# Optimization experiments

Measured on AMD Instinct MI355X. Metric: run time of the kernel, lower is better.

Reference implementation:

```python
import jax, jax.numpy as jnp
import numpy as np

QMAX = 127.0  # int8 symmetric
EPS = 1e-8

def _quant_dequant(v, axis):
    # symmetric int8 fake-quant along `axis` (per-row for weights, per-token for acts)
    scale = jnp.max(jnp.abs(v), axis=axis, keepdims=True) / QMAX
    scale = jnp.maximum(scale, EPS)
    q = jnp.clip(jnp.round(v / scale), -QMAX, QMAX)
    return q * scale

def _ste(v, axis):
    # straight-through estimator: identity gradient through quantization
    return v + jax.lax.stop_gradient(_quant_dequant(v, axis) - v)

def setup_inputs() -> dict:
    key = jax.random.key(0)
    k1, k2, k3 = jax.random.split(key, 3)
    H, I = 2048, 5632
    x = jax.random.normal(k1, (4, 2048, H), dtype=jnp.float32)
    # nn.Linear weight layout: [out_features, in_features]
    w_gate_up = jax.random.normal(k2, (2 * I, H), dtype=jnp.float32) * (H ** -0.5)
    w_down = jax.random.normal(k3, (H, I), dtype=jnp.float32) * (I ** -0.5)
    return {"x": x, "w_gate_up": w_gate_up, "w_down": w_down}

def reference(x, w_gate_up, w_down):
    I = w_down.shape[1]
    # QLinear #1: quantize act per-token, weight per-out-channel, dequant matmul
    xq = _ste(x, axis=-1)                       # [B,S,H]
    w1q = _ste(w_gate_up, axis=-1)              # [2I,H]
    gate_up = jnp.einsum('bsh,oh->bso', xq, w1q)  # [B,S,2I]
    gate, up = gate_up[..., :I], gate_up[..., I:]
    h = jax.nn.silu(gate) * up                  # SwiGLU, [B,S,I]
    # QLinear #2
    hq = _ste(h, axis=-1)
    w2q = _ste(w_down, axis=-1)                 # [H,I]
    return jnp.einsum('bsi,oi->bso', hq, w2q)   # [B,S,H]
```

## Files before the change

### kernel.cpp

```cpp
#include <hip/hip_runtime.h>
#include <hip/hip_bf16.h>
#include <stdint.h>

#define H_DIM 2048
#define I_DIM 5632
#define M_DIM 8192
#define N1_DIM (2 * I_DIM)
#define NBN1 (I_DIM / 128)
#define NPART (NBN1 * 4)

typedef __attribute__((ext_vector_type(4))) int i32x4;

__device__ __forceinline__ void gload16(const void* g, void* l) {
  __builtin_amdgcn_global_load_lds(
      reinterpret_cast<const __attribute__((address_space(1))) uint32_t*>(
          reinterpret_cast<uintptr_t>(g)),
      reinterpret_cast<__attribute__((address_space(3))) uint32_t*>(
          reinterpret_cast<uintptr_t>(l)),
      16, 0, 0);
}

__device__ __forceinline__ i32x4 ds_read128(uint32_t addr) {
  i32x4 d;
  asm volatile("s_mov_b32 m0, -1\n\tds_read_b128 %0, %1"
               : "=v"(d)
               : "v"(addr));
  return d;
}

#define MEMF() asm volatile("" ::: "memory")
#define BAR()                      \
  do {                             \
    MEMF();                        \
    __builtin_amdgcn_s_barrier();  \
    MEMF();                        \
  } while (0)
#define SCHEDB() __builtin_amdgcn_sched_barrier(0)

__global__ __launch_bounds__(256) void quant_rows_f32(
    const float* __restrict__ in, int8_t* __restrict__ q,
    float* __restrict__ scl, int rowlen) {
  const int row = blockIdx.x;
  const int tid = threadIdx.x;
  const float* rp = in + (size_t)row * rowlen;
  float m = 0.f;
  for (int i = tid * 4; i < rowlen; i += 1024) {
    const float4 v = *reinterpret_cast<const float4*>(rp + i);
    m = fmaxf(m, fmaxf(fmaxf(fabsf(v.x), fabsf(v.y)),
                       fmaxf(fabsf(v.z), fabsf(v.w))));
  }
#pragma unroll
  for (int o = 32; o; o >>= 1) m = fmaxf(m, __shfl_xor(m, o));
  __shared__ float wm[4];
  if ((tid & 63) == 0) wm[tid >> 6] = m;
  __syncthreads();
  m = fmaxf(fmaxf(wm[0], wm[1]), fmaxf(wm[2], wm[3]));
  const float scale = fmaxf(m / 127.0f, 1e-8f);
  const float inv = 1.0f / scale;
  if (tid == 0) scl[row] = scale;
  int8_t* qp = q + (size_t)row * rowlen;
  for (int i = tid * 4; i < rowlen; i += 1024) {
    const float4 v = *reinterpret_cast<const float4*>(rp + i);
    const int a = (int)rintf(fminf(fmaxf(v.x * inv, -127.f), 127.f));
    const int b = (int)rintf(fminf(fmaxf(v.y * inv, -127.f), 127.f));
    const int c = (int)rintf(fminf(fmaxf(v.z * inv, -127.f), 127.f));
    const int d = (int)rintf(fminf(fmaxf(v.w * inv, -127.f), 127.f));
    *reinterpret_cast<int*>(qp + i) =
        (a & 255) | ((b & 255) << 8) | ((c & 255) << 16) | (d << 24);
  }
}

__global__ __launch_bounds__(256) void quant_h_rows(
    const __hip_bfloat16* __restrict__ h, const float* __restrict__ hpart,
    int8_t* __restrict__ q, float* __restrict__ scl) {
  const int row = blockIdx.x;
  const int tid = threadIdx.x;
  float m = (tid < NPART) ? hpart[(size_t)row * NPART + tid] : 0.f;
#pragma unroll
  for (int o = 32; o; o >>= 1) m = fmaxf(m, __shfl_xor(m, o));
  __shared__ float wm[4];
  if ((tid & 63) == 0) wm[tid >> 6] = m;
  __syncthreads();
  m = fmaxf(fmaxf(wm[0], wm[1]), fmaxf(wm[2], wm[3]));
  const float scale = fmaxf(m / 127.0f, 1e-8f);
  const float inv = 1.0f / scale;
  if (tid == 0) scl[row] = scale;
  const __hip_bfloat16* rp = h + (size_t)row * I_DIM;
  int8_t* qp = q + (size_t)row * I_DIM;
  for (int i = tid * 8; i < I_DIM; i += 2048) {
    const uint4 v = *reinterpret_cast<const uint4*>(rp + i);
    const uint32_t w[4] = {v.x, v.y, v.z, v.w};
    int pk0 = 0, pk1 = 0;
#pragma unroll
    for (int j = 0; j < 8; ++j) {
      const float f =
          __uint_as_float(((w[j >> 1] >> ((j & 1) * 16)) & 0xffffu) << 16);
      const int qv = (int)rintf(fminf(fmaxf(f * inv, -127.f), 127.f));
      if (j < 4) pk0 |= (qv & 255) << ((j & 3) * 8);
      else       pk1 |= (qv & 255) << ((j & 3) * 8);
    }
    *reinterpret_cast<int2*>(qp + i) = make_int2(pk0, pk1);
  }
}

__global__ __launch_bounds__(512, 2) void gemm1_silu(
    const int8_t* __restrict__ qx, const float* __restrict__ sx,
    const int8_t* __restrict__ qw, const float* __restrict__ sw,
    __hip_bfloat16* __restrict__ h, float* __restrict__ hpart) {
  __shared__ int8_t lds[131072];
  const int tid = threadIdx.x;
  const int lane = tid & 63;
  const int wid = tid >> 6;
  const int wr = wid >> 2, wc = wid & 3;
  const int c16 = lane & 15, kq = lane >> 4, r7 = lane & 7, lr = lane >> 3;
  const int sslot = ((lane & 7) ^ lr) << 4;
  const int sl0 = (kq ^ r7) << 4;
  const int sl1 = ((4 + kq) ^ r7) << 4;

  const int nwg = gridDim.x;
  const int id = blockIdx.x;
  const int swz = (id & 7) * (nwg >> 3) + (id >> 3);
  const int bm = swz / NBN1, bn = swz % NBN1;

  const int xrow = wid * 8 + lr;
  const int fx = (xrow & ~31) | ((xrow & 15) << 1) | ((xrow >> 4) & 1);

  const size_t goffA = (size_t)(bm * 256 + xrow) * H_DIM + sslot;
  const size_t goffG = (size_t)(bn * 128 + fx) * H_DIM + sslot;
  const size_t goffU = goffG + (size_t)I_DIM * H_DIM;
  const int ldsAw = wid * 8 * 128;
  const int ldsBw = 65536 + wid * 8 * 128;

  const uint32_t L = (uint32_t)(uintptr_t)(void*)&lds[0];
  const uint32_t aB0 = L + (wr * 64 + c16) * 128 + sl0;
  const uint32_t aB1 = L + (wr * 64 + c16) * 128 + sl1;
  const uint32_t bB0 = L + 65536 + (wc * 32 + c16) * 128 + sl0;
  const uint32_t bB1 = L + 65536 + (wc * 32 + c16) * 128 + sl1;

  i32x4 acc[2][4][2][2] = {};

#define STAGE_A1(half, t)                                                      \
  do {                                                                         \
    const int _b = ((t) & 1) * 32768;                                          \
    _Pragma("unroll") for (int ld = 0; ld < 2; ++ld)                           \
        gload16(qx + goffA + (size_t)((half)*128 + ld * 64) * H_DIM +          \
                    (size_t)(t) * 128,                                         \
                lds + _b + ldsAw + ((half)*128 + ld * 64) * 128);              \
  } while (0)

#define STAGE_B1(half, t)                                                      \
  do {                                                                         \
    const int _b = ((t) & 1) * 32768;                                          \
    const int8_t* _s = (half) ? (qw + goffU) : (qw + goffG);                   \
    _Pragma("unroll") for (int ld = 0; ld < 2; ++ld)                           \
        gload16(_s + (size_t)(ld * 64) * H_DIM + (size_t)(t) * 128,            \
                lds + _b + ldsBw + ((half)*128 + ld * 64) * 128);              \
  } while (0)

#define RD_A(MH)                                                               \
  do {                                                                         \
    _Pragma("unroll") for (int m = 0; m < 4; ++m) {                            \
      a[MH][m][0] = ds_read128(ab0 + (MH)*16384 + m * 2048);                   \
      a[MH][m][1] = ds_read128(ab1 + (MH)*16384 + m * 2048);                   \
    }                                                                          \
  } while (0)

#define RD_B(NH)                                                               \
  do {                                                                         \
    _Pragma("unroll") for (int n = 0; n < 2; ++n) {                            \
      b[NH][n][0] = ds_read128(bb0 + (NH)*16384 + n * 2048);                   \
      b[NH][n][1] = ds_read128(bb1 + (NH)*16384 + n * 2048);                   \
    }                                                                          \
  } while (0)

#define MFMA_Q(MH, NH)                                                         \
  do {                                                                         \
    __builtin_amdgcn_s_setprio(1);                                             \
    _Pragma("unroll") for (int kk = 0; kk < 2; ++kk)                           \
        _Pragma("unroll") for (int m = 0; m < 4; ++m)                          \
            _Pragma("unroll") for (int n = 0; n < 2; ++n) acc[MH][m][NH][n] =  \
        __builtin_amdgcn_mfma_i32_16x16x64_i8(a[MH][m][kk], b[NH][n][kk],      \
                                              acc[MH][m][NH][n], 0, 0, 0);     \
    __builtin_amdgcn_s_setprio(0);                                             \
  } while (0)

  const int KT = H_DIM / 128;
  STAGE_A1(0, 0); STAGE_B1(0, 0); STAGE_A1(1, 0); STAGE_B1(1, 0);
  STAGE_A1(0, 1); STAGE_B1(0, 1);
  asm volatile("s_waitcnt vmcnt(4)" ::: "memory");
  BAR();

#pragma unroll 1
  for (int t = 0; t < KT; ++t) {
    const int cb = (t & 1) * 32768;
    const uint32_t ab0 = aB0 + cb, ab1 = aB1 + cb;
    const uint32_t bb0 = bB0 + cb, bb1 = bB1 + cb;
    i32x4 a[2][4][2], b[2][2][2];
    RD_B(0); RD_A(0); RD_B(1);
    MEMF();
    if (t + 1 < KT) { STAGE_A1(1, t + 1); STAGE_B1(1, t + 1); }
    BAR();
    asm volatile("s_waitcnt lgkmcnt(4)" ::: "memory");
    SCHEDB();
    MFMA_Q(0, 0);
    asm volatile("s_waitcnt lgkmcnt(0)" ::: "memory");
    SCHEDB();
    MFMA_Q(0, 1);
    BAR();
    RD_A(1);
    MEMF();
    if (t + 2 < KT) { STAGE_A1(0, t + 2); STAGE_B1(0, t + 2); }
    BAR();
    asm volatile("s_waitcnt lgkmcnt(0)" ::: "memory");
    SCHEDB();
    MFMA_Q(1, 0);
    MFMA_Q(1, 1);
    if (t + 2 < KT) asm volatile("s_waitcnt vmcnt(4)" ::: "memory");
    else            asm volatile("s_waitcnt vmcnt(0)" ::: "memory");
    BAR();
  }

  const int row0 = bm * 256 + wr * 64 + kq * 4;
  const int colb = bn * 128 + wc * 32 + 2 * c16;
#pragma unroll
  for (int mh = 0; mh < 2; ++mh) {
#pragma unroll
    for (int m = 0; m < 4; ++m) {
#pragma unroll
      for (int r = 0; r < 4; ++r) {
        const int row = row0 + mh * 128 + m * 16 + r;
        const float sxr = sx[row];
        float hv[2];
#pragma unroll
        for (int n = 0; n < 2; ++n) {
          const int col = colb + n;
          const float g = (float)acc[mh][m][0][n][r] * (sxr * sw[col]);
          const float u = (float)acc[mh][m][1][n][r] * (sxr * sw[I_DIM + col]);
          hv[n] = g / (1.f + __expf(-g)) * u;
        }
        const uint32_t p0 = __bfloat16_as_ushort(__float2bfloat16(hv[0]));
        const uint32_t p1 = __bfloat16_as_ushort(__float2bfloat16(hv[1]));
        *reinterpret_cast<uint32_t*>(&h[(size_t)row * I_DIM + colb]) =
            p0 | (p1 << 16);
        float rmax = fmaxf(fabsf(hv[0]), fabsf(hv[1]));
#pragma unroll
        for (int o = 1; o < 16; o <<= 1)
          rmax = fmaxf(rmax, __shfl_xor(rmax, o));
        if (c16 == 0)
          hpart[(size_t)row * NPART + bn * 4 + wc] = rmax;
      }
    }
  }
}

__global__ __launch_bounds__(512, 2) void gemm2(
    const int8_t* __restrict__ qh, const float* __restrict__ sh,
    const int8_t* __restrict__ qw, const float* __restrict__ sw,
    float* __restrict__ out) {
  __shared__ int8_t lds[131072];
  const int tid = threadIdx.x;
  const int lane = tid & 63;
  const int wid = tid >> 6;
  const int wr = wid >> 2, wc = wid & 3;
  const int c16 = lane & 15, kq = lane >> 4, r7 = lane & 7, lr = lane >> 3;
  const int sslot = ((lane & 7) ^ lr) << 4;
  const int sl0 = (kq ^ r7) << 4;
  const int sl1 = ((4 + kq) ^ r7) << 4;

  const int nwg = gridDim.x;
  const int id = blockIdx.x;
  const int swz = (id & 7) * (nwg >> 3) + (id >> 3);
  const int NBN = H_DIM / 256;
  const int bm = swz / NBN, bn = swz % NBN;

  const size_t goffA = (size_t)(bm * 256 + wid * 8 + lr) * I_DIM + sslot;
  const size_t goffB = (size_t)(bn * 256 + wid * 8 + lr) * I_DIM + sslot;
  const int ldsAw = wid * 8 * 128;
  const int ldsBw = 65536 + wid * 8 * 128;

  const uint32_t L = (uint32_t)(uintptr_t)(void*)&lds[0];
  const uint32_t aB0 = L + (wr * 64 + c16) * 128 + sl0;
  const uint32_t aB1 = L + (wr * 64 + c16) * 128 + sl1;
  const uint32_t bB0 = L + 65536 + (wc * 32 + c16) * 128 + sl0;
  const uint32_t bB1 = L + 65536 + (wc * 32 + c16) * 128 + sl1;

  i32x4 acc[2][4][2][2] = {};

#define STAGE_A2(half, t)                                                      \
  do {                                                                         \
    const int _b = ((t) & 1) * 32768;                                          \
    _Pragma("unroll") for (int ld = 0; ld < 2; ++ld)                           \
        gload16(qh + goffA + (size_t)((half)*128 + ld * 64) * I_DIM +          \
                    (size_t)(t) * 128,                                         \
                lds + _b + ldsAw + ((half)*128 + ld * 64) * 128);              \
  } while (0)

#define STAGE_B2(half, t)                                                      \
  do {                                                                         \
    const int _b = ((t) & 1) * 32768;                                          \
    _Pragma("unroll") for (int ld = 0; ld < 2; ++ld)                           \
        gload16(qw + goffB + (size_t)((half)*128 + ld * 64) * I_DIM +          \
                    (size_t)(t) * 128,                                         \
                lds + _b + ldsBw + ((half)*128 + ld * 64) * 128);              \
  } while (0)

  const int KT = I_DIM / 128;
  STAGE_A2(0, 0); STAGE_B2(0, 0); STAGE_A2(1, 0); STAGE_B2(1, 0);
  STAGE_A2(0, 1); STAGE_B2(0, 1);
  asm volatile("s_waitcnt vmcnt(4)" ::: "memory");
  BAR();

#pragma unroll 1
  for (int t = 0; t < KT; ++t) {
    const int cb = (t & 1) * 32768;
    const uint32_t ab0 = aB0 + cb, ab1 = aB1 + cb;
    const uint32_t bb0 = bB0 + cb, bb1 = bB1 + cb;
    i32x4 a[2][4][2], b[2][2][2];
    RD_B(0); RD_A(0); RD_B(1);
    MEMF();
    if (t + 1 < KT) { STAGE_A2(1, t + 1); STAGE_B2(1, t + 1); }
    BAR();
    asm volatile("s_waitcnt lgkmcnt(4)" ::: "memory");
    SCHEDB();
    MFMA_Q(0, 0);
    asm volatile("s_waitcnt lgkmcnt(0)" ::: "memory");
    SCHEDB();
    MFMA_Q(0, 1);
    BAR();
    RD_A(1);
    MEMF();
    if (t + 2 < KT) { STAGE_A2(0, t + 2); STAGE_B2(0, t + 2); }
    BAR();
    asm volatile("s_waitcnt lgkmcnt(0)" ::: "memory");
    SCHEDB();
    MFMA_Q(1, 0);
    MFMA_Q(1, 1);
    if (t + 2 < KT) asm volatile("s_waitcnt vmcnt(4)" ::: "memory");
    else            asm volatile("s_waitcnt vmcnt(0)" ::: "memory");
    BAR();
  }

  const int row0 = bm * 256 + wr * 64 + kq * 4;
  const int col0 = bn * 256 + wc * 32 + c16;
#pragma unroll
  for (int mh = 0; mh < 2; ++mh) {
#pragma unroll
    for (int m = 0; m < 4; ++m) {
#pragma unroll
      for (int r = 0; r < 4; ++r) {
        const int row = row0 + mh * 128 + m * 16 + r;
        const float shr = sh[row];
#pragma unroll
        for (int nh = 0; nh < 2; ++nh) {
#pragma unroll
          for (int n = 0; n < 2; ++n) {
            const int col = col0 + nh * 128 + n * 16;
            out[(size_t)row * H_DIM + col] =
                (float)acc[mh][m][nh][n][r] * (shr * sw[col]);
          }
        }
      }
    }
  }
}

extern "C" void kernel_launch(void* const* d_in, const int* in_sizes, int n_in,
                              void* d_out, int out_size, void* d_ws, size_t ws_size,
                              hipStream_t stream) {
  (void)in_sizes; (void)n_in; (void)out_size; (void)ws_size;
  const float* x  = (const float*)d_in[0];
  const float* w1 = (const float*)d_in[1];
  const float* w2 = (const float*)d_in[2];
  float* out = (float*)d_out;

  size_t off = 0;
  auto alloc = [&](size_t n) {
    void* p = (char*)d_ws + off;
    off += (n + 255) & ~(size_t)255;
    return p;
  };
  int8_t* qx  = (int8_t*)alloc((size_t)M_DIM * H_DIM);
  int8_t* qw1 = (int8_t*)alloc((size_t)N1_DIM * H_DIM);
  int8_t* qw2 = (int8_t*)alloc((size_t)H_DIM * I_DIM);
  int8_t* qh  = (int8_t*)alloc((size_t)M_DIM * I_DIM);
  __hip_bfloat16* hb = (__hip_bfloat16*)alloc((size_t)M_DIM * I_DIM * 2);
  float* sx    = (float*)alloc((size_t)M_DIM * 4);
  float* sw1   = (float*)alloc((size_t)N1_DIM * 4);
  float* sw2   = (float*)alloc((size_t)H_DIM * 4);
  float* shs   = (float*)alloc((size_t)M_DIM * 4);
  float* hpart = (float*)alloc((size_t)M_DIM * NPART * 4);

  quant_rows_f32<<<M_DIM, 256, 0, stream>>>(x, qx, sx, H_DIM);
  quant_rows_f32<<<N1_DIM, 256, 0, stream>>>(w1, qw1, sw1, H_DIM);
  quant_rows_f32<<<H_DIM, 256, 0, stream>>>(w2, qw2, sw2, I_DIM);
  gemm1_silu<<<(M_DIM / 256) * NBN1, 512, 0, stream>>>(
      qx, sx, qw1, sw1, hb, hpart);
  quant_h_rows<<<M_DIM, 256, 0, stream>>>(hb, hpart, qh, shs);
  gemm2<<<(M_DIM / 256) * (H_DIM / 256), 512, 0, stream>>>(
      qh, shs, qw2, sw2, out);
}
```

Before: 408.6 us.

## Software-pipeline LDS fragment reads across k-tiles in int8 GEMM main loops

```diff
diff --git a/kernel.cpp b/kernel.cpp
--- a/kernel.cpp
+++ b/kernel.cpp
@@ -103,6 +103,77 @@
   }
 }
 
+#define RD_A(MH, BUF)                                                          \
+  do {                                                                         \
+    _Pragma("unroll") for (int m = 0; m < 4; ++m) {                            \
+      a[MH][m][0] = ds_read128(aB0 + (BUF) + (MH)*16384 + m * 2048);           \
+      a[MH][m][1] = ds_read128(aB1 + (BUF) + (MH)*16384 + m * 2048);           \
+    }                                                                          \
+  } while (0)
+
+#define RD_B(NH, BUF)                                                          \
+  do {                                                                         \
+    _Pragma("unroll") for (int n = 0; n < 2; ++n) {                            \
+      b[NH][n][0] = ds_read128(bB0 + (BUF) + (NH)*16384 + n * 2048);           \
+      b[NH][n][1] = ds_read128(bB1 + (BUF) + (NH)*16384 + n * 2048);           \
+    }                                                                          \
+  } while (0)
+
+#define MFMA_Q(MH, NH)                                                         \
+  do {                                                                         \
+    __builtin_amdgcn_s_setprio(1);                                             \
+    _Pragma("unroll") for (int kk = 0; kk < 2; ++kk)                           \
+        _Pragma("unroll") for (int m = 0; m < 4; ++m)                          \
+            _Pragma("unroll") for (int n = 0; n < 2; ++n) acc[MH][m][NH][n] =  \
+        __builtin_amdgcn_mfma_i32_16x16x64_i8(a[MH][m][kk], b[NH][n][kk],      \
+                                              acc[MH][m][NH][n], 0, 0, 0);     \
+    __builtin_amdgcn_s_setprio(0);                                             \
+  } while (0)
+
+#define KTILE_BODY(SA, SB)                                                     \
+  do {                                                                         \
+    const int cb = (t & 1) * 32768;                                            \
+    const int nb = cb ^ 32768;                                                 \
+                                                                      \
+    SCHEDB();                                                                  \
+    RD_B(1, cb);                                                               \
+    MEMF();                                                                    \
+    if (t + 1 < KT) SA(1, t + 1);                                              \
+    asm volatile("s_waitcnt lgkmcnt(4)" ::: "memory");                         \
+    SCHEDB();                                                                  \
+    MFMA_Q(0, 0);                                                              \
+    BAR();                                                                     \
+                                                                      \
+    SCHEDB();                                                                  \
+    RD_A(1, cb);                                                               \
+    MEMF();                                                                    \
+    if (t + 1 < KT) SB(1, t + 1);                                              \
+    asm volatile("s_waitcnt lgkmcnt(8)" ::: "memory");                         \
+    SCHEDB();                                                                  \
+    MFMA_Q(0, 1);                                                              \
+    BAR();                                                                     \
+                                                                      \
+    SCHEDB();                                                                  \
+    if (t + 2 < KT) SA(0, t + 2);                                              \
+    asm volatile("s_waitcnt lgkmcnt(0)" ::: "memory");                         \
+    SCHEDB();                                                                  \
+    MFMA_Q(1, 0);                                                              \
+    if (t + 2 < KT) asm volatile("s_waitcnt vmcnt(6)" ::: "memory");           \
+    else            asm volatile("s_waitcnt vmcnt(0)" ::: "memory");           \
+    BAR();                                                                     \
+                                                                      \
+    SCHEDB();                                                                  \
+    if (t + 1 < KT) { RD_A(0, nb); RD_B(0, nb); }                              \
+    MEMF();                                                                    \
+    if (t + 2 < KT) SB(0, t + 2);                                              \
+    MFMA_Q(1, 1);                                                              \
+    if (t + 1 < KT) {                                                          \
+      if (t + 2 < KT) asm volatile("s_waitcnt vmcnt(4)" ::: "memory");         \
+      else            asm volatile("s_waitcnt vmcnt(0)" ::: "memory");         \
+    }                                                                          \
+    BAR();                                                                     \
+  } while (0)
+
 __global__ __launch_bounds__(512, 2) void gemm1_silu(
     const int8_t* __restrict__ qx, const float* __restrict__ sx,
     const int8_t* __restrict__ qw, const float* __restrict__ sw,
@@ -138,6 +209,7 @@
   const uint32_t bB1 = L + 65536 + (wc * 32 + c16) * 128 + sl1;
 
   i32x4 acc[2][4][2][2] = {};
+  i32x4 a[2][4][2], b[2][2][2];
 
 #define STAGE_A1(half, t)                                                      \
   do {                                                                         \
@@ -157,67 +229,17 @@
                 lds + _b + ldsBw + ((half)*128 + ld * 64) * 128);              \
   } while (0)
 
-#define RD_A(MH)                                                               \
-  do {                                                                         \
-    _Pragma("unroll") for (int m = 0; m < 4; ++m) {                            \
-      a[MH][m][0] = ds_read128(ab0 + (MH)*16384 + m * 2048);                   \
-      a[MH][m][1] = ds_read128(ab1 + (MH)*16384 + m * 2048);                   \
-    }                                                                          \
-  } while (0)
-
-#define RD_B(NH)                                                               \
-  do {                                                                         \
-    _Pragma("unroll") for (int n = 0; n < 2; ++n) {                            \
-      b[NH][n][0] = ds_read128(bb0 + (NH)*16384 + n * 2048);                   \
-      b[NH][n][1] = ds_read128(bb1 + (NH)*16384 + n * 2048);                   \
-    }                                                                          \
-  } while (0)
-
-#define MFMA_Q(MH, NH)                                                         \
-  do {                                                                         \
-    __builtin_amdgcn_s_setprio(1);                                             \
-    _Pragma("unroll") for (int kk = 0; kk < 2; ++kk)                           \
-        _Pragma("unroll") for (int m = 0; m < 4; ++m)                          \
-            _Pragma("unroll") for (int n = 0; n < 2; ++n) acc[MH][m][NH][n] =  \
-        __builtin_amdgcn_mfma_i32_16x16x64_i8(a[MH][m][kk], b[NH][n][kk],      \
-                                              acc[MH][m][NH][n], 0, 0, 0);     \
-    __builtin_amdgcn_s_setprio(0);                                             \
-  } while (0)
-
   const int KT = H_DIM / 128;
   STAGE_A1(0, 0); STAGE_B1(0, 0); STAGE_A1(1, 0); STAGE_B1(1, 0);
   STAGE_A1(0, 1); STAGE_B1(0, 1);
   asm volatile("s_waitcnt vmcnt(4)" ::: "memory");
   BAR();
+  RD_A(0, 0); RD_B(0, 0);
+  MEMF();
 
 #pragma unroll 1
   for (int t = 0; t < KT; ++t) {
-    const int cb = (t & 1) * 32768;
-    const uint32_t ab0 = aB0 + cb, ab1 = aB1 + cb;
-    const uint32_t bb0 = bB0 + cb, bb1 = bB1 + cb;
-    i32x4 a[2][4][2], b[2][2][2];
-    RD_B(0); RD_A(0); RD_B(1);
-    MEMF();
-    if (t + 1 < KT) { STAGE_A1(1, t + 1); STAGE_B1(1, t + 1); }
-    BAR();
-    asm volatile("s_waitcnt lgkmcnt(4)" ::: "memory");
-    SCHEDB();
-    MFMA_Q(0, 0);
-    asm volatile("s_waitcnt lgkmcnt(0)" ::: "memory");
-    SCHEDB();
-    MFMA_Q(0, 1);
-    BAR();
-    RD_A(1);
-    MEMF();
-    if (t + 2 < KT) { STAGE_A1(0, t + 2); STAGE_B1(0, t + 2); }
-    BAR();
-    asm volatile("s_waitcnt lgkmcnt(0)" ::: "memory");
-    SCHEDB();
-    MFMA_Q(1, 0);
-    MFMA_Q(1, 1);
-    if (t + 2 < KT) asm volatile("s_waitcnt vmcnt(4)" ::: "memory");
-    else            asm volatile("s_waitcnt vmcnt(0)" ::: "memory");
-    BAR();
+    KTILE_BODY(STAGE_A1, STAGE_B1);
   }
 
   const int row0 = bm * 256 + wr * 64 + kq * 4;
@@ -285,6 +307,7 @@
   const uint32_t bB1 = L + 65536 + (wc * 32 + c16) * 128 + sl1;
 
   i32x4 acc[2][4][2][2] = {};
+  i32x4 a[2][4][2], b[2][2][2];
 
 #define STAGE_A2(half, t)                                                      \
   do {                                                                         \
@@ -309,35 +332,12 @@
   STAGE_A2(0, 1); STAGE_B2(0, 1);
   asm volatile("s_waitcnt vmcnt(4)" ::: "memory");
   BAR();
+  RD_A(0, 0); RD_B(0, 0);
+  MEMF();
 
 #pragma unroll 1
   for (int t = 0; t < KT; ++t) {
-    const int cb = (t & 1) * 32768;
-    const uint32_t ab0 = aB0 + cb, ab1 = aB1 + cb;
-    const uint32_t bb0 = bB0 + cb, bb1 = bB1 + cb;
-    i32x4 a[2][4][2], b[2][2][2];
-    RD_B(0); RD_A(0); RD_B(1);
-    MEMF();
-    if (t + 1 < KT) { STAGE_A2(1, t + 1); STAGE_B2(1, t + 1); }
-    BAR();
-    asm volatile("s_waitcnt lgkmcnt(4)" ::: "memory");
-    SCHEDB();
-    MFMA_Q(0, 0);
-    asm volatile("s_waitcnt lgkmcnt(0)" ::: "memory");
-    SCHEDB();
-    MFMA_Q(0, 1);
-    BAR();
-    RD_A(1);
-    MEMF();
-    if (t + 2 < KT) { STAGE_A2(0, t + 2); STAGE_B2(0, t + 2); }
-    BAR();
-    asm volatile("s_waitcnt lgkmcnt(0)" ::: "memory");
-    SCHEDB();
-    MFMA_Q(1, 0);
-    MFMA_Q(1, 1);
-    if (t + 2 < KT) asm volatile("s_waitcnt vmcnt(4)" ::: "memory");
-    else            asm volatile("s_waitcnt vmcnt(0)" ::: "memory");
-    BAR();
+    KTILE_BODY(STAGE_A2, STAGE_B2);
   }
 
   const int row0 = bm * 256 + wr * 64 + kq * 4;
```

After: 403.3 us. About the same (-1.3%).

## Make gemm1 persistent with cross-tile prefetch and restage both GEMM main loops

Applied to the files above, without the earlier changes.

```diff
diff --git a/kernel.cpp b/kernel.cpp
--- a/kernel.cpp
+++ b/kernel.cpp
@@ -8,6 +8,8 @@
 #define N1_DIM (2 * I_DIM)
 #define NBN1 (I_DIM / 128)
 #define NPART (NBN1 * 4)
+#define NT1 ((M_DIM / 256) * NBN1)
+#define G1_GRID 256
 
 typedef __attribute__((ext_vector_type(4))) int i32x4;
 
@@ -103,6 +105,33 @@
   }
 }
 
+#define RD_A(MH, BUF)                                                          \
+  do {                                                                         \
+    _Pragma("unroll") for (int m = 0; m < 4; ++m) {                            \
+      a[MH][m][0] = ds_read128(aB0 + (BUF) + (MH)*16384 + m * 2048);           \
+      a[MH][m][1] = ds_read128(aB1 + (BUF) + (MH)*16384 + m * 2048);           \
+    }                                                                          \
+  } while (0)
+
+#define RD_B(NH, BUF)                                                          \
+  do {                                                                         \
+    _Pragma("unroll") for (int n = 0; n < 2; ++n) {                            \
+      b[NH][n][0] = ds_read128(bB0 + (BUF) + (NH)*16384 + n * 2048);           \
+      b[NH][n][1] = ds_read128(bB1 + (BUF) + (NH)*16384 + n * 2048);           \
+    }                                                                          \
+  } while (0)
+
+#define MFMA_Q(MH, NH)                                                         \
+  do {                                                                         \
+    __builtin_amdgcn_s_setprio(1);                                             \
+    _Pragma("unroll") for (int kk = 0; kk < 2; ++kk)                           \
+        _Pragma("unroll") for (int m = 0; m < 4; ++m)                          \
+            _Pragma("unroll") for (int n = 0; n < 2; ++n) acc[MH][m][NH][n] =  \
+        __builtin_amdgcn_mfma_i32_16x16x64_i8(a[MH][m][kk], b[NH][n][kk],      \
+                                              acc[MH][m][NH][n], 0, 0, 0);     \
+    __builtin_amdgcn_s_setprio(0);                                             \
+  } while (0)
+
 __global__ __launch_bounds__(512, 2) void gemm1_silu(
     const int8_t* __restrict__ qx, const float* __restrict__ sx,
     const int8_t* __restrict__ qw, const float* __restrict__ sw,
@@ -117,17 +146,9 @@
   const int sl0 = (kq ^ r7) << 4;
   const int sl1 = ((4 + kq) ^ r7) << 4;
 
-  const int nwg = gridDim.x;
-  const int id = blockIdx.x;
-  const int swz = (id & 7) * (nwg >> 3) + (id >> 3);
-  const int bm = swz / NBN1, bn = swz % NBN1;
-
   const int xrow = wid * 8 + lr;
   const int fx = (xrow & ~31) | ((xrow & 15) << 1) | ((xrow >> 4) & 1);
 
-  const size_t goffA = (size_t)(bm * 256 + xrow) * H_DIM + sslot;
-  const size_t goffG = (size_t)(bn * 128 + fx) * H_DIM + sslot;
-  const size_t goffU = goffG + (size_t)I_DIM * H_DIM;
   const int ldsAw = wid * 8 * 128;
   const int ldsBw = 65536 + wid * 8 * 128;
 
@@ -137,119 +158,148 @@
   const uint32_t bB0 = L + 65536 + (wc * 32 + c16) * 128 + sl0;
   const uint32_t bB1 = L + 65536 + (wc * 32 + c16) * 128 + sl1;
 
-  i32x4 acc[2][4][2][2] = {};
-
-#define STAGE_A1(half, t)                                                      \
-  do {                                                                         \
-    const int _b = ((t) & 1) * 32768;                                          \
+  const int KT = H_DIM / 128;
+
+#define STG_A(P, half, vv)                                                     \
+  do {                                                                         \
+    const int _b = ((vv) & 1) * 32768;                                         \
+    const int _t = (vv) & 15;                                                  \
     _Pragma("unroll") for (int ld = 0; ld < 2; ++ld)                           \
-        gload16(qx + goffA + (size_t)((half)*128 + ld * 64) * H_DIM +          \
-                    (size_t)(t) * 128,                                         \
+        gload16((P) + (size_t)((half)*128 + ld * 64) * H_DIM +                 \
+                    (size_t)_t * 128,                                          \
                 lds + _b + ldsAw + ((half)*128 + ld * 64) * 128);              \
   } while (0)
 
-#define STAGE_B1(half, t)                                                      \
-  do {                                                                         \
-    const int _b = ((t) & 1) * 32768;                                          \
-    const int8_t* _s = (half) ? (qw + goffU) : (qw + goffG);                   \
+#define STG_B(P, half, vv)                                                     \
+  do {                                                                         \
+    const int _b = ((vv) & 1) * 32768;                                         \
+    const int _t = (vv) & 15;                                                  \
     _Pragma("unroll") for (int ld = 0; ld < 2; ++ld)                           \
-        gload16(_s + (size_t)(ld * 64) * H_DIM + (size_t)(t) * 128,            \
+        gload16((P) + (size_t)(ld * 64) * H_DIM + (size_t)_t * 128,            \
                 lds + _b + ldsBw + ((half)*128 + ld * 64) * 128);              \
   } while (0)
 
-#define RD_A(MH)                                                               \
-  do {                                                                         \
-    _Pragma("unroll") for (int m = 0; m < 4; ++m) {                            \
-      a[MH][m][0] = ds_read128(ab0 + (MH)*16384 + m * 2048);                   \
-      a[MH][m][1] = ds_read128(ab1 + (MH)*16384 + m * 2048);                   \
-    }                                                                          \
-  } while (0)
-
-#define RD_B(NH)                                                               \
-  do {                                                                         \
-    _Pragma("unroll") for (int n = 0; n < 2; ++n) {                            \
-      b[NH][n][0] = ds_read128(bb0 + (NH)*16384 + n * 2048);                   \
-      b[NH][n][1] = ds_read128(bb1 + (NH)*16384 + n * 2048);                   \
-    }                                                                          \
-  } while (0)
-
-#define MFMA_Q(MH, NH)                                                         \
-  do {                                                                         \
-    __builtin_amdgcn_s_setprio(1);                                             \
-    _Pragma("unroll") for (int kk = 0; kk < 2; ++kk)                           \
-        _Pragma("unroll") for (int m = 0; m < 4; ++m)                          \
-            _Pragma("unroll") for (int n = 0; n < 2; ++n) acc[MH][m][NH][n] =  \
-        __builtin_amdgcn_mfma_i32_16x16x64_i8(a[MH][m][kk], b[NH][n][kk],      \
-                                              acc[MH][m][NH][n], 0, 0, 0);     \
-    __builtin_amdgcn_s_setprio(0);                                             \
-  } while (0)
-
-  const int KT = H_DIM / 128;
-  STAGE_A1(0, 0); STAGE_B1(0, 0); STAGE_A1(1, 0); STAGE_B1(1, 0);
-  STAGE_A1(0, 1); STAGE_B1(0, 1);
+  int v = blockIdx.x;
+  int swz = (v & 7) * (NT1 / 8) + (v >> 3);
+  int bm_c = swz / NBN1, bn_c = swz % NBN1;
+  const int8_t* pAc = qx + (size_t)(bm_c * 256 + xrow) * H_DIM + sslot;
+  const int8_t* pGc = qw + (size_t)(bn_c * 128 + fx) * H_DIM + sslot;
+  const int8_t* pUc = pGc + (size_t)I_DIM * H_DIM;
+
+  i32x4 acc[2][4][2][2];
+  i32x4 a[2][4][2], b[2][2][2];
+
+  STG_A(pAc, 0, 0); STG_B(pGc, 0, 0);
+  STG_A(pAc, 1, 0); STG_B(pUc, 1, 0);
+  STG_A(pAc, 0, 1); STG_B(pGc, 0, 1);
   asm volatile("s_waitcnt vmcnt(4)" ::: "memory");
   BAR();
 
 #pragma unroll 1
-  for (int t = 0; t < KT; ++t) {
-    const int cb = (t & 1) * 32768;
-    const uint32_t ab0 = aB0 + cb, ab1 = aB1 + cb;
-    const uint32_t bb0 = bB0 + cb, bb1 = bB1 + cb;
-    i32x4 a[2][4][2], b[2][2][2];
-    RD_B(0); RD_A(0); RD_B(1);
+  for (; v < NT1; v += G1_GRID) {
+    const bool last = (v + G1_GRID >= NT1);
+    const int vn = last ? v : v + G1_GRID;
+    const int swzn = (vn & 7) * (NT1 / 8) + (vn >> 3);
+    const int bm_n = swzn / NBN1, bn_n = swzn % NBN1;
+    const int8_t* pAn = qx + (size_t)(bm_n * 256 + xrow) * H_DIM + sslot;
+    const int8_t* pGn = qw + (size_t)(bn_n * 128 + fx) * H_DIM + sslot;
+    const int8_t* pUn = pGn + (size_t)I_DIM * H_DIM;
+
+    RD_A(0, 0); RD_B(0, 0);
     MEMF();
-    if (t + 1 < KT) { STAGE_A1(1, t + 1); STAGE_B1(1, t + 1); }
-    BAR();
-    asm volatile("s_waitcnt lgkmcnt(4)" ::: "memory");
-    SCHEDB();
-    MFMA_Q(0, 0);
-    asm volatile("s_waitcnt lgkmcnt(0)" ::: "memory");
-    SCHEDB();
-    MFMA_Q(0, 1);
-    BAR();
-    RD_A(1);
-    MEMF();
-    if (t + 2 < KT) { STAGE_A1(0, t + 2); STAGE_B1(0, t + 2); }
-    BAR();
-    asm volatile("s_waitcnt lgkmcnt(0)" ::: "memory");
-    SCHEDB();
-    MFMA_Q(1, 0);
-    MFMA_Q(1, 1);
-    if (t + 2 < KT) asm volatile("s_waitcnt vmcnt(4)" ::: "memory");
-    else            asm volatile("s_waitcnt vmcnt(0)" ::: "memory");
-    BAR();
-  }
-
-  const int row0 = bm * 256 + wr * 64 + kq * 4;
-  const int colb = bn * 128 + wc * 32 + 2 * c16;
-#pragma unroll
-  for (int mh = 0; mh < 2; ++mh) {
-#pragma unroll
-    for (int m = 0; m < 4; ++m) {
-#pragma unroll
-      for (int r = 0; r < 4; ++r) {
-        const int row = row0 + mh * 128 + m * 16 + r;
-        const float sxr = sx[row];
-        float hv[2];
-#pragma unroll
-        for (int n = 0; n < 2; ++n) {
-          const int col = colb + n;
-          const float g = (float)acc[mh][m][0][n][r] * (sxr * sw[col]);
-          const float u = (float)acc[mh][m][1][n][r] * (sxr * sw[I_DIM + col]);
-          hv[n] = g / (1.f + __expf(-g)) * u;
+
+#pragma unroll
+    for (int mh = 0; mh < 2; ++mh)
+#pragma unroll
+      for (int m = 0; m < 4; ++m)
+#pragma unroll
+        for (int nh = 0; nh < 2; ++nh)
+#pragma unroll
+          for (int n = 0; n < 2; ++n) acc[mh][m][nh][n] = i32x4{0, 0, 0, 0};
+
+#pragma unroll 1
+    for (int t = 0; t < KT; ++t) {
+      const int cb = (t & 1) * 32768;
+      const int nb = cb ^ 32768;
+      SCHEDB();
+      RD_B(1, cb);
+      MEMF();
+      if (t + 1 < KT)      STG_A(pAc, 1, t + 1);
+      else if (!last)      STG_A(pAn, 1, t + 1);
+      asm volatile("s_waitcnt lgkmcnt(4)" ::: "memory");
+      SCHEDB();
+      MFMA_Q(0, 0);
+      BAR();
+      SCHEDB();
+      RD_A(1, cb);
+      MEMF();
+      if (t + 1 < KT)      STG_B(pUc, 1, t + 1);
+      else if (!last)      STG_B(pUn, 1, t + 1);
+      asm volatile("s_waitcnt lgkmcnt(8)" ::: "memory");
+      SCHEDB();
+      MFMA_Q(0, 1);
+      BAR();
+      SCHEDB();
+      if (t + 2 < KT)      STG_A(pAc, 0, t + 2);
+      else if (!last)      STG_A(pAn, 0, t + 2);
+      asm volatile("s_waitcnt lgkmcnt(0)" ::: "memory");
+      SCHEDB();
+      MFMA_Q(1, 0);
+      if (t + 2 < KT || !last)
+        asm volatile("s_waitcnt vmcnt(6)" ::: "memory");
+      else
+        asm volatile("s_waitcnt vmcnt(0)" ::: "memory");
+      BAR();
+      SCHEDB();
+      if (t + 1 < KT) { RD_A(0, nb); RD_B(0, nb); }
+      MEMF();
+      if (t + 2 < KT)      STG_B(pGc, 0, t + 2);
+      else if (!last)      STG_B(pGn, 0, t + 2);
+      MFMA_Q(1, 1);
+      if (t + 1 < KT || !last) {
+        if (t + 2 < KT || !last)
+          asm volatile("s_waitcnt vmcnt(4)" ::: "memory");
+        else
+          asm volatile("s_waitcnt vmcnt(0)" ::: "memory");
+      }
+      BAR();
+    }
+
+    const int row0 = bm_c * 256 + wr * 64 + kq * 4;
+    const int colb = bn_c * 128 + wc * 32 + 2 * c16;
+#pragma unroll
+    for (int mh = 0; mh < 2; ++mh) {
+#pragma unroll
+      for (int m = 0; m < 4; ++m) {
+#pragma unroll
+        for (int r = 0; r < 4; ++r) {
+          const int row = row0 + mh * 128 + m * 16 + r;
+          const float sxr = sx[row];
+          float hv[2];
+#pragma unroll
+          for (int n = 0; n < 2; ++n) {
+            const int col = colb + n;
+            const float g = (float)acc[mh][m][0][n][r] * (sxr * sw[col]);
+            const float u =
+                (float)acc[mh][m][1][n][r] * (sxr * sw[I_DIM + col]);
+            hv[n] = g / (1.f + __expf(-g)) * u;
+          }
+          const uint32_t p0 = __bfloat16_as_ushort(__float2bfloat16(hv[0]));
+          const uint32_t p1 = __bfloat16_as_ushort(__float2bfloat16(hv[1]));
+          *reinterpret_cast<uint32_t*>(&h[(size_t)row * I_DIM + colb]) =
+              p0 | (p1 << 16);
+          float rmax = fmaxf(fabsf(hv[0]), fabsf(hv[1]));
+#pragma unroll
+          for (int o = 1; o < 16; o <<= 1)
+            rmax = fmaxf(rmax, __shfl_xor(rmax, o));
+          if (c16 == 0)
+            hpart[(size_t)row * NPART + bn_c * 4 + wc] = rmax;
         }
-        const uint32_t p0 = __bfloat16_as_ushort(__float2bfloat16(hv[0]));
-        const uint32_t p1 = __bfloat16_as_ushort(__float2bfloat16(hv[1]));
-        *reinterpret_cast<uint32_t*>(&h[(size_t)row * I_DIM + colb]) =
-            p0 | (p1 << 16);
-        float rmax = fmaxf(fabsf(hv[0]), fabsf(hv[1]));
-#pragma unroll
-        for (int o = 1; o < 16; o <<= 1)
-          rmax = fmaxf(rmax, __shfl_xor(rmax, o));
-        if (c16 == 0)
-          hpart[(size_t)row * NPART + bn * 4 + wc] = rmax;
       }
     }
+
+    bm_c = bm_n; bn_c = bn_n;
+    pAc = pAn; pGc = pGn; pUc = pUn;
   }
 }
 
@@ -285,6 +335,7 @@
   const uint32_t bB1 = L + 65536 + (wc * 32 + c16) * 128 + sl1;
 
   i32x4 acc[2][4][2][2] = {};
+  i32x4 a[2][4][2], b[2][2][2];
 
 #define STAGE_A2(half, t)                                                      \
   do {                                                                         \
@@ -309,34 +360,46 @@
   STAGE_A2(0, 1); STAGE_B2(0, 1);
   asm volatile("s_waitcnt vmcnt(4)" ::: "memory");
   BAR();
+  RD_A(0, 0); RD_B(0, 0);
+  MEMF();
 
 #pragma unroll 1
   for (int t = 0; t < KT; ++t) {
     const int cb = (t & 1) * 32768;
-    const uint32_t ab0 = aB0 + cb, ab1 = aB1 + cb;
-    const uint32_t bb0 = bB0 + cb, bb1 = bB1 + cb;
-    i32x4 a[2][4][2], b[2][2][2];
-    RD_B(0); RD_A(0); RD_B(1);
+    const int nb = cb ^ 32768;
+    SCHEDB();
+    RD_B(1, cb);
     MEMF();
-    if (t + 1 < KT) { STAGE_A2(1, t + 1); STAGE_B2(1, t + 1); }
+    if (t + 1 < KT) STAGE_A2(1, t + 1);
+    asm volatile("s_waitcnt lgkmcnt(4)" ::: "memory");
+    SCHEDB();
+    MFMA_Q(0, 0);
     BAR();
-    asm volatile("s_waitcnt lgkmcnt(4)" ::: "memory");
-    SCHEDB();
-    MFMA_Q(0, 0);
-    asm volatile("s_waitcnt lgkmcnt(0)" ::: "memory");
+    SCHEDB();
+    RD_A(1, cb);
+    MEMF();
+    if (t + 1 < KT) STAGE_B2(1, t + 1);
+    asm volatile("s_waitcnt lgkmcnt(8)" ::: "memory");
     SCHEDB();
     MFMA_Q(0, 1);
     BAR();
-    RD_A(1);
+    SCHEDB();
+    if (t + 2 < KT) STAGE_A2(0, t + 2);
+    asm volatile("s_waitcnt lgkmcnt(0)" ::: "memory");
+    SCHEDB();
+    MFMA_Q(1, 0);
+    if (t + 2 < KT) asm volatile("s_waitcnt vmcnt(6)" ::: "memory");
+    else            asm volatile("s_waitcnt vmcnt(0)" ::: "memory");
+    BAR();
+    SCHEDB();
+    if (t + 1 < KT) { RD_A(0, nb); RD_B(0, nb); }
     MEMF();
-    if (t + 2 < KT) { STAGE_A2(0, t + 2); STAGE_B2(0, t + 2); }
-    BAR();
-    asm volatile("s_waitcnt lgkmcnt(0)" ::: "memory");
-    SCHEDB();
-    MFMA_Q(1, 0);
+    if (t + 2 < KT) STAGE_B2(0, t + 2);
     MFMA_Q(1, 1);
-    if (t + 2 < KT) asm volatile("s_waitcnt vmcnt(4)" ::: "memory");
-    else            asm volatile("s_waitcnt vmcnt(0)" ::: "memory");
+    if (t + 1 < KT) {
+      if (t + 2 < KT) asm volatile("s_waitcnt vmcnt(4)" ::: "memory");
+      else            asm volatile("s_waitcnt vmcnt(0)" ::: "memory");
+    }
     BAR();
   }
 
@@ -393,8 +456,7 @@
   quant_rows_f32<<<M_DIM, 256, 0, stream>>>(x, qx, sx, H_DIM);
   quant_rows_f32<<<N1_DIM, 256, 0, stream>>>(w1, qw1, sw1, H_DIM);
   quant_rows_f32<<<H_DIM, 256, 0, stream>>>(w2, qw2, sw2, I_DIM);
-  gemm1_silu<<<(M_DIM / 256) * NBN1, 512, 0, stream>>>(
-      qx, sx, qw1, sw1, hb, hpart);
+  gemm1_silu<<<G1_GRID, 512, 0, stream>>>(qx, sx, qw1, sw1, hb, hpart);
   quant_h_rows<<<M_DIM, 256, 0, stream>>>(hb, hpart, qh, shs);
   gemm2<<<(M_DIM / 256) * (H_DIM / 256), 512, 0, stream>>>(
       qh, shs, qw2, sw2, out);
```

Result: no change. 411.6 us (+0.7%).
